# Kernel optimization log

Hardware: AMD Instinct MI355X
Metric: run time of the kernel (lower is better)

The kernel has to match this reference:

```python
import jax, jax.numpy as jnp
import numpy as np

N_NODES = 50000
N_EDGES = 800000
DIM = 128
N_GRAPHS = 64


def gcn_layer(x, edge_index, W, b):
    """PyG GCNConv: symmetric-normalized A+I aggregation then linear."""
    n = x.shape[0]
    loop = jnp.arange(n)
    row = jnp.concatenate([edge_index[0], loop])  # source nodes (+ self loops)
    col = jnp.concatenate([edge_index[1], loop])  # target nodes (+ self loops)
    deg = jax.ops.segment_sum(jnp.ones_like(col, dtype=x.dtype), col, num_segments=n)
    dis = jnp.where(deg > 0, jax.lax.rsqrt(deg), 0.0)
    norm = dis[row] * dis[col]  # [E+N]
    h = x @ W  # [N, out]
    out = jax.ops.segment_sum(h[row] * norm[:, None], col, num_segments=n)
    return out + b


def setup_inputs() -> dict:
    key = jax.random.key(0)
    ks = jax.random.split(key, 10)
    x = jax.random.normal(ks[0], (N_NODES, DIM), dtype=jnp.float32)
    edge_index = jax.random.randint(ks[1], (2, N_EDGES), 0, N_NODES, dtype=jnp.int64)
    batch = jnp.sort(jax.random.randint(ks[2], (N_NODES,), 0, N_GRAPHS, dtype=jnp.int64))
    W1 = jax.random.normal(ks[3], (DIM, DIM), dtype=jnp.float32) * 0.05
    W2 = jax.random.normal(ks[4], (DIM, DIM), dtype=jnp.float32) * 0.05
    W3 = jax.random.normal(ks[5], (DIM, DIM), dtype=jnp.float32) * 0.05
    b1 = jnp.zeros((DIM,), jnp.float32)
    b2 = jnp.zeros((DIM,), jnp.float32)
    b3 = jnp.zeros((DIM,), jnp.float32)
    return {"x": x, "edge_index": edge_index, "batch": batch,
            "W1": W1, "b1": b1, "W2": W2, "b2": b2, "W3": W3, "b3": b3}


def reference(x, edge_index, batch, W1, b1, W2, b2, W3, b3):
    h = jax.nn.relu(gcn_layer(x, edge_index, W1, b1))
    h = jax.nn.relu(gcn_layer(h, edge_index, W2, b2))
    h = jax.nn.relu(gcn_layer(h, edge_index, W3, b3))
    # global mean pool over graphs
    s = jax.ops.segment_sum(h, batch, num_segments=N_GRAPHS)
    cnt = jax.ops.segment_sum(jnp.ones((h.shape[0],), h.dtype), batch, num_segments=N_GRAPHS)
    return s / jnp.maximum(cnt, 1.0)[:, None]
```

## Files before the change

### kernel.cpp

```cpp
#include <hip/hip_runtime.h>
#include <hip/hip_bf16.h>

#define DIM 128
#define N_GRAPHS 64
#define SSTR 136

typedef __attribute__((ext_vector_type(4))) float f32x4;
typedef __attribute__((ext_vector_type(8))) short s16x8;


__device__ __forceinline__ short bf16h(float f) {
    return __builtin_bit_cast(short, __float2bfloat16(f));
}
__device__ __forceinline__ float bf16f(unsigned short h) {
    unsigned u = ((unsigned)h) << 16;
    return __builtin_bit_cast(float, u);
}

__global__ void k_rank4(const int4* __restrict__ col4, int* __restrict__ cnt,
                        int4* __restrict__ pos4, int e4) {
    int i = blockIdx.x * blockDim.x + threadIdx.x;
    if (i >= e4) return;
    int4 c = col4[i];
    int4 p;
    p.x = atomicAdd(&cnt[c.x], 1);
    p.y = atomicAdd(&cnt[c.y], 1);
    p.z = atomicAdd(&cnt[c.z], 1);
    p.w = atomicAdd(&cnt[c.w], 1);
    pos4[i] = p;
}

__global__ __launch_bounds__(256) void k_bsum(const int* __restrict__ cnt,
                                              int* __restrict__ bsum, int n) {
    __shared__ int s[256];
    int t = threadIdx.x;
    int i = blockIdx.x * 256 + t;
    s[t] = (i < n) ? cnt[i] : 0;
    __syncthreads();
    for (int o = 128; o > 0; o >>= 1) {
        if (t < o) s[t] += s[t + o];
        __syncthreads();
    }
    if (t == 0) bsum[blockIdx.x] = s[0];
}

__global__ __launch_bounds__(256) void k_bscan(const int* __restrict__ bsum,
                                               int* __restrict__ bbase, int nb) {
    __shared__ int s[256];
    int t = threadIdx.x;
    int v = (t < nb) ? bsum[t] : 0;
    s[t] = v;
    __syncthreads();
    for (int o = 1; o < 256; o <<= 1) {
        int u = (t >= o) ? s[t - o] : 0;
        __syncthreads();
        s[t] += u;
        __syncthreads();
    }
    if (t < nb) bbase[t] = s[t] - v;
}

__global__ __launch_bounds__(256) void k_bfinal(const int* __restrict__ cnt,
        const int* __restrict__ bbase, int* __restrict__ rowptr,
        float* __restrict__ dis, int n, int e) {
    __shared__ int s[256];
    int t = threadIdx.x;
    int i = blockIdx.x * 256 + t;
    int v = (i < n) ? cnt[i] : 0;
    s[t] = v;
    __syncthreads();
    for (int o = 1; o < 256; o <<= 1) {
        int u = (t >= o) ? s[t - o] : 0;
        __syncthreads();
        s[t] += u;
        __syncthreads();
    }
    if (i < n) {
        rowptr[i] = s[t] - v + bbase[blockIdx.x];
        dis[i] = rsqrtf(1.0f + (float)v);
        if (i == n - 1) rowptr[n] = e;
    }
}

__global__ void k_scat4(const int4* __restrict__ row4, const int4* __restrict__ col4,
                        const int4* __restrict__ pos4, const int* __restrict__ rowptr,
                        int* __restrict__ csr_src, int e4) {
    int i = blockIdx.x * blockDim.x + threadIdx.x;
    if (i >= e4) return;
    int4 r = row4[i];
    int4 c = col4[i];
    int4 p = pos4[i];
    csr_src[rowptr[c.x] + p.x] = r.x;
    csr_src[rowptr[c.y] + p.y] = r.y;
    csr_src[rowptr[c.z] + p.z] = r.z;
    csr_src[rowptr[c.w] + p.w] = r.w;
}


__global__ void k_cvt(const float* __restrict__ x, unsigned short* __restrict__ xb,
                      int total4) {
    int i = blockIdx.x * blockDim.x + threadIdx.x;
    if (i >= total4) return;
    float4 v = ((const float4*)x)[i];
    ushort4 o = {(unsigned short)bf16h(v.x), (unsigned short)bf16h(v.y),
                 (unsigned short)bf16h(v.z), (unsigned short)bf16h(v.w)};
    ((ushort4*)xb)[i] = o;
}


__global__ __launch_bounds__(256) void k_gcn_agg_bf(const unsigned short* __restrict__ in,
        const int* __restrict__ csr_src, const int* __restrict__ rowptr,
        const float* __restrict__ dis, float* __restrict__ agg, int n) {
    int wid = (blockIdx.x * blockDim.x + threadIdx.x) >> 6;
    if (wid >= n) return;
    int lane = threadIdx.x & 63;
    const int coff = lane * 2;
    float d = dis[wid];
    float dd = d * d;
    ushort2 sv = *(const ushort2*)&in[(size_t)wid * DIM + coff];
    float2 acc = {bf16f(sv.x) * dd, bf16f(sv.y) * dd};
    int p = rowptr[wid], p1 = rowptr[wid + 1];
    for (; p + 3 < p1; p += 4) {
        int s0 = csr_src[p], s1 = csr_src[p + 1], s2 = csr_src[p + 2], s3 = csr_src[p + 3];
        float w0 = d * dis[s0], w1 = d * dis[s1], w2 = d * dis[s2], w3 = d * dis[s3];
        ushort2 v0 = *(const ushort2*)&in[(size_t)s0 * DIM + coff];
        ushort2 v1 = *(const ushort2*)&in[(size_t)s1 * DIM + coff];
        ushort2 v2 = *(const ushort2*)&in[(size_t)s2 * DIM + coff];
        ushort2 v3 = *(const ushort2*)&in[(size_t)s3 * DIM + coff];
        acc.x += bf16f(v0.x) * w0; acc.y += bf16f(v0.y) * w0;
        acc.x += bf16f(v1.x) * w1; acc.y += bf16f(v1.y) * w1;
        acc.x += bf16f(v2.x) * w2; acc.y += bf16f(v2.y) * w2;
        acc.x += bf16f(v3.x) * w3; acc.y += bf16f(v3.y) * w3;
    }
    for (; p < p1; p++) {
        int s = csr_src[p];
        float w = d * dis[s];
        ushort2 v = *(const ushort2*)&in[(size_t)s * DIM + coff];
        acc.x += bf16f(v.x) * w;
        acc.y += bf16f(v.y) * w;
    }
    *(float2*)&agg[(size_t)wid * DIM + coff] = acc;
}

__global__ __launch_bounds__(256) void k_wprep3(
        const float* __restrict__ W1, const float* __restrict__ W2,
        const float* __restrict__ W3,
        unsigned short* __restrict__ hi1, unsigned short* __restrict__ lo1,
        unsigned short* __restrict__ hi2, unsigned short* __restrict__ lo2,
        unsigned short* __restrict__ hi3, unsigned short* __restrict__ lo3) {
    int m = blockIdx.x >> 6;
    int i = (blockIdx.x & 63) * 256 + threadIdx.x;
    const float* W = (m == 0) ? W1 : (m == 1) ? W2 : W3;
    unsigned short* hi = (m == 0) ? hi1 : (m == 1) ? hi2 : hi3;
    unsigned short* lo = (m == 0) ? lo1 : (m == 1) ? lo2 : lo3;
    int k = i >> 7, c = i & 127;
    float w = W[i];
    short h = bf16h(w);
    short l = bf16h(w - bf16f((unsigned short)h));
    hi[c * DIM + k] = (unsigned short)h;
    lo[c * DIM + k] = (unsigned short)l;
}


__global__ __launch_bounds__(256) void k_mm_mfma(
        const float* __restrict__ A, const unsigned short* __restrict__ wt_hi,
        const unsigned short* __restrict__ wt_lo, const float* __restrict__ bias,
        unsigned short* __restrict__ out, int n) {
    __shared__ unsigned short sAh[64 * SSTR];
    __shared__ unsigned short sAl[64 * SSTR];
    int tid = threadIdx.x;
    int wave = tid >> 6, lane = tid & 63;
    int r0b = blockIdx.x * 64;

    {
        int subrow = tid >> 5;
        int colb = (tid & 31) * 4;
        const float4* A4 = (const float4*)A;
#pragma unroll
        for (int j = 0; j < 8; j++) {
            int row = j * 8 + subrow;
            int rowg = r0b + row;
            int rowc = rowg < n ? rowg : (n - 1);
            float4 v = A4[(size_t)rowc * 32 + (colb >> 2)];
            short h0 = bf16h(v.x), h1 = bf16h(v.y), h2 = bf16h(v.z), h3 = bf16h(v.w);
            short l0 = bf16h(v.x - bf16f((unsigned short)h0));
            short l1 = bf16h(v.y - bf16f((unsigned short)h1));
            short l2 = bf16h(v.z - bf16f((unsigned short)h2));
            short l3 = bf16h(v.w - bf16f((unsigned short)h3));
            ushort4 hv = {(unsigned short)h0, (unsigned short)h1,
                          (unsigned short)h2, (unsigned short)h3};
            ushort4 lv = {(unsigned short)l0, (unsigned short)l1,
                          (unsigned short)l2, (unsigned short)l3};
            *(ushort4*)&sAh[row * SSTR + colb] = hv;
            *(ushort4*)&sAl[row * SSTR + colb] = lv;
        }
    }
    __syncthreads();

    int lrow = lane & 15;
    int lk = lane >> 4;
    bool full = (r0b + 64 <= n);

#pragma unroll
    for (int cti = 0; cti < 2; cti++) {
        int ct = wave * 2 + cti;
        int col = ct * 16 + lrow;
        const unsigned short* bh_base = wt_hi + (size_t)col * DIM + lk * 8;
        const unsigned short* bl_base = wt_lo + (size_t)col * DIM + lk * 8;
        s16x8 bh[4], bl[4];
#pragma unroll
        for (int ks = 0; ks < 4; ks++) {
            bh[ks] = *(const s16x8*)(bh_base + ks * 32);
            bl[ks] = *(const s16x8*)(bl_base + ks * 32);
        }
        float bcol = bias[col];

#pragma unroll
        for (int rt = 0; rt < 4; rt++) {
            const unsigned short* ah_base = &sAh[(rt * 16 + lrow) * SSTR + lk * 8];
            const unsigned short* al_base = &sAl[(rt * 16 + lrow) * SSTR + lk * 8];
            s16x8 ah[4], al[4];
#pragma unroll
            for (int ks = 0; ks < 4; ks++) {
                ah[ks] = *(const s16x8*)(ah_base + ks * 32);
                al[ks] = *(const s16x8*)(al_base + ks * 32);
            }
            f32x4 c = {0.f, 0.f, 0.f, 0.f};
#pragma unroll
            for (int ks = 0; ks < 4; ks++) {
                c = __builtin_amdgcn_mfma_f32_16x16x32_bf16(ah[ks], bh[ks], c, 0, 0, 0);
                c = __builtin_amdgcn_mfma_f32_16x16x32_bf16(al[ks], bh[ks], c, 0, 0, 0);
                c = __builtin_amdgcn_mfma_f32_16x16x32_bf16(ah[ks], bl[ks], c, 0, 0, 0);
            }
            int rbase = r0b + rt * 16 + lk * 4;
            if (full) {
#pragma unroll
                for (int reg = 0; reg < 4; reg++) {
                    float v = c[reg] + bcol;
                    v = v > 0.f ? v : 0.f;
                    out[(size_t)(rbase + reg) * DIM + col] = (unsigned short)bf16h(v);
                }
            } else {
#pragma unroll
                for (int reg = 0; reg < 4; reg++) {
                    if (rbase + reg < n) {
                        float v = c[reg] + bcol;
                        v = v > 0.f ? v : 0.f;
                        out[(size_t)(rbase + reg) * DIM + col] = (unsigned short)bf16h(v);
                    }
                }
            }
        }
    }
}


__global__ __launch_bounds__(256) void k_pool_part(const unsigned short* __restrict__ h,
        const int* __restrict__ batch, float* __restrict__ part, int n) {
    int g = blockIdx.x >> 4, s = blockIdx.x & 15;
    int lo = 0, hi = n;
    while (lo < hi) { int m = (lo + hi) >> 1; if (batch[m] < g) lo = m + 1; else hi = m; }
    int start = lo;
    int lo2 = start, hi2 = n;
    while (lo2 < hi2) { int m = (lo2 + hi2) >> 1; if (batch[m] < g + 1) lo2 = m + 1; else hi2 = m; }
    int end = lo2;

    int t = threadIdx.x;
    int wave = t >> 6, lane = t & 63;
    float2 acc = {0.f, 0.f};
    for (int r = start + s + 16 * wave; r < end; r += 64) {
        ushort2 v = *(const ushort2*)&h[(size_t)r * DIM + lane * 2];
        acc.x += bf16f(v.x); acc.y += bf16f(v.y);
    }
    __shared__ float2 red[4][64];
    red[wave][lane] = acc;
    __syncthreads();
    if (t < 64) {
        float2 s0 = red[0][t], s1 = red[1][t], s2 = red[2][t], s3 = red[3][t];
        float2 o;
        o.x = s0.x + s1.x + s2.x + s3.x;
        o.y = s0.y + s1.y + s2.y + s3.y;
        *(float2*)&part[(size_t)blockIdx.x * DIM + t * 2] = o;
    }
}

__global__ __launch_bounds__(128) void k_pool_fin(const float* __restrict__ part,
        const int* __restrict__ batch, float* __restrict__ out, int n) {
    int g = blockIdx.x, c = threadIdx.x;
    int lo = 0, hi = n;
    while (lo < hi) { int m = (lo + hi) >> 1; if (batch[m] < g) lo = m + 1; else hi = m; }
    int start = lo;
    int lo2 = start, hi2 = n;
    while (lo2 < hi2) { int m = (lo2 + hi2) >> 1; if (batch[m] < g + 1) lo2 = m + 1; else hi2 = m; }
    int end = lo2;

    float s = 0.f;
#pragma unroll
    for (int k = 0; k < 16; k++) s += part[(size_t)(g * 16 + k) * DIM + c];
    float cnt = (float)(end - start);
    cnt = cnt > 1.f ? cnt : 1.f;
    out[g * DIM + c] = s / cnt;
}


extern "C" void kernel_launch(void* const* d_in, const int* in_sizes, int n_in,
                              void* d_out, int out_size, void* d_ws, size_t ws_size,
                              hipStream_t stream) {
    const float* x  = (const float*)d_in[0];
    const int*   ei = (const int*)d_in[1];
    const int*   batch = (const int*)d_in[2];
    const float* W1 = (const float*)d_in[3];
    const float* b1 = (const float*)d_in[4];
    const float* W2 = (const float*)d_in[5];
    const float* b2 = (const float*)d_in[6];
    const float* W3 = (const float*)d_in[7];
    const float* b3 = (const float*)d_in[8];

    int n = in_sizes[0] / DIM;
    int e = in_sizes[1] / 2;
    const int* erow = ei;
    const int* ecol = ei + e;
    int e4 = e / 4;
    int nb = (n + 255) / 256;

    char* ws = (char*)d_ws;
    size_t off = 0;
    auto alloc = [&](size_t bytes) -> void* {
        void* p = (void*)(ws + off);
        off += (bytes + 255) & ~(size_t)255;
        return p;
    };
    float* dis     = (float*)alloc((size_t)n * 4);
    int*   rowptr  = (int*)alloc((size_t)(n + 1) * 4);
    int*   csr_src = (int*)alloc((size_t)e * 4);
    float* agg     = (float*)alloc((size_t)n * DIM * 4);
    unsigned short* xb    = (unsigned short*)alloc((size_t)n * DIM * 2);
    unsigned short* hbufA = (unsigned short*)alloc((size_t)n * DIM * 2);
    unsigned short* hbufB = (unsigned short*)alloc((size_t)n * DIM * 2);
    unsigned short* wt_hi1 = (unsigned short*)alloc(DIM * DIM * 2);
    unsigned short* wt_lo1 = (unsigned short*)alloc(DIM * DIM * 2);
    unsigned short* wt_hi2 = (unsigned short*)alloc(DIM * DIM * 2);
    unsigned short* wt_lo2 = (unsigned short*)alloc(DIM * DIM * 2);
    unsigned short* wt_hi3 = (unsigned short*)alloc(DIM * DIM * 2);
    unsigned short* wt_lo3 = (unsigned short*)alloc(DIM * DIM * 2);
    float* part    = (float*)alloc((size_t)1024 * DIM * 4);
    int*   pos     = (int*)alloc((size_t)e * 4);
    int* cnt    = (int*)agg;
    int* bsum   = ((int*)agg) + n;
    int* bbase  = ((int*)agg) + n + 256;

    hipMemsetAsync(cnt, 0, (size_t)n * 4, stream);
    k_rank4<<<(e4 + 255) / 256, 256, 0, stream>>>((const int4*)ecol, cnt, (int4*)pos, e4);
    k_bsum<<<nb, 256, 0, stream>>>(cnt, bsum, n);
    k_bscan<<<1, 256, 0, stream>>>(bsum, bbase, nb);
    k_bfinal<<<nb, 256, 0, stream>>>(cnt, bbase, rowptr, dis, n, e);
    k_scat4<<<(e4 + 255) / 256, 256, 0, stream>>>((const int4*)erow, (const int4*)ecol,
                                                  (const int4*)pos, rowptr, csr_src, e4);

    int total4 = n * DIM / 4;
    k_cvt<<<(total4 + 255) / 256, 256, 0, stream>>>(x, xb, total4);
    k_wprep3<<<192, 256, 0, stream>>>(W1, W2, W3, wt_hi1, wt_lo1, wt_hi2, wt_lo2,
                                      wt_hi3, wt_lo3);

    dim3 aggGrid(((size_t)n * 64 + 255) / 256);
    dim3 mmGrid((n + 63) / 64);

    k_gcn_agg_bf<<<aggGrid, 256, 0, stream>>>(xb, csr_src, rowptr, dis, agg, n);
    k_mm_mfma<<<mmGrid, 256, 0, stream>>>(agg, wt_hi1, wt_lo1, b1, hbufA, n);
    k_gcn_agg_bf<<<aggGrid, 256, 0, stream>>>(hbufA, csr_src, rowptr, dis, agg, n);
    k_mm_mfma<<<mmGrid, 256, 0, stream>>>(agg, wt_hi2, wt_lo2, b2, hbufB, n);
    k_gcn_agg_bf<<<aggGrid, 256, 0, stream>>>(hbufB, csr_src, rowptr, dis, agg, n);
    k_mm_mfma<<<mmGrid, 256, 0, stream>>>(agg, wt_hi3, wt_lo3, b3, hbufA, n);

    k_pool_part<<<1024, 256, 0, stream>>>(hbufA, batch, part, n);
    k_pool_fin<<<N_GRAPHS, 128, 0, stream>>>(part, batch, (float*)d_out, n);
}
```

Before: 257.2 us.

## Reorder GCN layer to transform-then-aggregate with bf16 intermediates

Each layer now multiplies by W before the sparse aggregation instead of after. The aggregation kernel takes over the bias, ReLU and bf16 store, and the matmul reads bf16 inputs directly. This removes the fp32 agg buffer and its write and read, and drops one of the three split-bf16 MFMA passes since A is now bf16 only. In exchange, the matmul output Y is rounded to bf16 before aggregation, which adds precision loss.

```diff
diff --git a/kernel.cpp b/kernel.cpp
--- a/kernel.cpp
+++ b/kernel.cpp
@@ -107,10 +107,98 @@
     ((ushort4*)xb)[i] = o;
 }
 
+__global__ __launch_bounds__(256) void k_wprep3(
+        const float* __restrict__ W1, const float* __restrict__ W2,
+        const float* __restrict__ W3,
+        unsigned short* __restrict__ hi1, unsigned short* __restrict__ lo1,
+        unsigned short* __restrict__ hi2, unsigned short* __restrict__ lo2,
+        unsigned short* __restrict__ hi3, unsigned short* __restrict__ lo3) {
+    int m = blockIdx.x >> 6;
+    int i = (blockIdx.x & 63) * 256 + threadIdx.x;
+    const float* W = (m == 0) ? W1 : (m == 1) ? W2 : W3;
+    unsigned short* hi = (m == 0) ? hi1 : (m == 1) ? hi2 : hi3;
+    unsigned short* lo = (m == 0) ? lo1 : (m == 1) ? lo2 : lo3;
+    int k = i >> 7, c = i & 127;
+    float w = W[i];
+    short h = bf16h(w);
+    short l = bf16h(w - bf16f((unsigned short)h));
+    hi[c * DIM + k] = (unsigned short)h;
+    lo[c * DIM + k] = (unsigned short)l;
+}
+
+
+__global__ __launch_bounds__(256) void k_mm2(
+        const unsigned short* __restrict__ A, const unsigned short* __restrict__ wt_hi,
+        const unsigned short* __restrict__ wt_lo, unsigned short* __restrict__ out, int n) {
+    __shared__ unsigned short sA[64 * SSTR];
+    int tid = threadIdx.x;
+    int wave = tid >> 6, lane = tid & 63;
+    int r0b = blockIdx.x * 64;
+
+    for (int c = tid; c < 1024; c += 256) {
+        int row = c >> 4;
+        int cc = (c & 15) * 8;
+        int rowg = r0b + row;
+        int rowc = rowg < n ? rowg : (n - 1);
+        s16x8 v = *(const s16x8*)&A[(size_t)rowc * DIM + cc];
+        *(s16x8*)&sA[row * SSTR + cc] = v;
+    }
+    __syncthreads();
+
+    int lrow = lane & 15;
+    int lk = lane >> 4;
+    bool full = (r0b + 64 <= n);
+
+#pragma unroll
+    for (int cti = 0; cti < 2; cti++) {
+        int ct = wave * 2 + cti;
+        int col = ct * 16 + lrow;
+        const unsigned short* bh_base = wt_hi + (size_t)col * DIM + lk * 8;
+        const unsigned short* bl_base = wt_lo + (size_t)col * DIM + lk * 8;
+        s16x8 bh[4], bl[4];
+#pragma unroll
+        for (int ks = 0; ks < 4; ks++) {
+            bh[ks] = *(const s16x8*)(bh_base + ks * 32);
+            bl[ks] = *(const s16x8*)(bl_base + ks * 32);
+        }
+
+#pragma unroll
+        for (int rt = 0; rt < 4; rt++) {
+            const unsigned short* a_base = &sA[(rt * 16 + lrow) * SSTR + lk * 8];
+            s16x8 a[4];
+#pragma unroll
+            for (int ks = 0; ks < 4; ks++) {
+                a[ks] = *(const s16x8*)(a_base + ks * 32);
+            }
+            f32x4 c = {0.f, 0.f, 0.f, 0.f};
+#pragma unroll
+            for (int ks = 0; ks < 4; ks++) {
+                c = __builtin_amdgcn_mfma_f32_16x16x32_bf16(a[ks], bh[ks], c, 0, 0, 0);
+                c = __builtin_amdgcn_mfma_f32_16x16x32_bf16(a[ks], bl[ks], c, 0, 0, 0);
+            }
+            int rbase = r0b + rt * 16 + lk * 4;
+            if (full) {
+#pragma unroll
+                for (int reg = 0; reg < 4; reg++) {
+                    out[(size_t)(rbase + reg) * DIM + col] = (unsigned short)bf16h(c[reg]);
+                }
+            } else {
+#pragma unroll
+                for (int reg = 0; reg < 4; reg++) {
+                    if (rbase + reg < n) {
+                        out[(size_t)(rbase + reg) * DIM + col] = (unsigned short)bf16h(c[reg]);
+                    }
+                }
+            }
+        }
+    }
+}
+
 
 __global__ __launch_bounds__(256) void k_gcn_agg_bf(const unsigned short* __restrict__ in,
         const int* __restrict__ csr_src, const int* __restrict__ rowptr,
-        const float* __restrict__ dis, float* __restrict__ agg, int n) {
+        const float* __restrict__ dis, const float* __restrict__ bias,
+        unsigned short* __restrict__ hout, int n) {
     int wid = (blockIdx.x * blockDim.x + threadIdx.x) >> 6;
     if (wid >= n) return;
     int lane = threadIdx.x & 63;
@@ -139,119 +227,13 @@
         acc.x += bf16f(v.x) * w;
         acc.y += bf16f(v.y) * w;
     }
-    *(float2*)&agg[(size_t)wid * DIM + coff] = acc;
-}
-
-__global__ __launch_bounds__(256) void k_wprep3(
-        const float* __restrict__ W1, const float* __restrict__ W2,
-        const float* __restrict__ W3,
-        unsigned short* __restrict__ hi1, unsigned short* __restrict__ lo1,
-        unsigned short* __restrict__ hi2, unsigned short* __restrict__ lo2,
-        unsigned short* __restrict__ hi3, unsigned short* __restrict__ lo3) {
-    int m = blockIdx.x >> 6;
-    int i = (blockIdx.x & 63) * 256 + threadIdx.x;
-    const float* W = (m == 0) ? W1 : (m == 1) ? W2 : W3;
-    unsigned short* hi = (m == 0) ? hi1 : (m == 1) ? hi2 : hi3;
-    unsigned short* lo = (m == 0) ? lo1 : (m == 1) ? lo2 : lo3;
-    int k = i >> 7, c = i & 127;
-    float w = W[i];
-    short h = bf16h(w);
-    short l = bf16h(w - bf16f((unsigned short)h));
-    hi[c * DIM + k] = (unsigned short)h;
-    lo[c * DIM + k] = (unsigned short)l;
-}
-
-
-__global__ __launch_bounds__(256) void k_mm_mfma(
-        const float* __restrict__ A, const unsigned short* __restrict__ wt_hi,
-        const unsigned short* __restrict__ wt_lo, const float* __restrict__ bias,
-        unsigned short* __restrict__ out, int n) {
-    __shared__ unsigned short sAh[64 * SSTR];
-    __shared__ unsigned short sAl[64 * SSTR];
-    int tid = threadIdx.x;
-    int wave = tid >> 6, lane = tid & 63;
-    int r0b = blockIdx.x * 64;
-
-    {
-        int subrow = tid >> 5;
-        int colb = (tid & 31) * 4;
-        const float4* A4 = (const float4*)A;
-#pragma unroll
-        for (int j = 0; j < 8; j++) {
-            int row = j * 8 + subrow;
-            int rowg = r0b + row;
-            int rowc = rowg < n ? rowg : (n - 1);
-            float4 v = A4[(size_t)rowc * 32 + (colb >> 2)];
-            short h0 = bf16h(v.x), h1 = bf16h(v.y), h2 = bf16h(v.z), h3 = bf16h(v.w);
-            short l0 = bf16h(v.x - bf16f((unsigned short)h0));
-            short l1 = bf16h(v.y - bf16f((unsigned short)h1));
-            short l2 = bf16h(v.z - bf16f((unsigned short)h2));
-            short l3 = bf16h(v.w - bf16f((unsigned short)h3));
-            ushort4 hv = {(unsigned short)h0, (unsigned short)h1,
-                          (unsigned short)h2, (unsigned short)h3};
-            ushort4 lv = {(unsigned short)l0, (unsigned short)l1,
-                          (unsigned short)l2, (unsigned short)l3};
-            *(ushort4*)&sAh[row * SSTR + colb] = hv;
-            *(ushort4*)&sAl[row * SSTR + colb] = lv;
-        }
-    }
-    __syncthreads();
-
-    int lrow = lane & 15;
-    int lk = lane >> 4;
-    bool full = (r0b + 64 <= n);
-
-#pragma unroll
-    for (int cti = 0; cti < 2; cti++) {
-        int ct = wave * 2 + cti;
-        int col = ct * 16 + lrow;
-        const unsigned short* bh_base = wt_hi + (size_t)col * DIM + lk * 8;
-        const unsigned short* bl_base = wt_lo + (size_t)col * DIM + lk * 8;
-        s16x8 bh[4], bl[4];
-#pragma unroll
-        for (int ks = 0; ks < 4; ks++) {
-            bh[ks] = *(const s16x8*)(bh_base + ks * 32);
-            bl[ks] = *(const s16x8*)(bl_base + ks * 32);
-        }
-        float bcol = bias[col];
-
-#pragma unroll
-        for (int rt = 0; rt < 4; rt++) {
-            const unsigned short* ah_base = &sAh[(rt * 16 + lrow) * SSTR + lk * 8];
-            const unsigned short* al_base = &sAl[(rt * 16 + lrow) * SSTR + lk * 8];
-            s16x8 ah[4], al[4];
-#pragma unroll
-            for (int ks = 0; ks < 4; ks++) {
-                ah[ks] = *(const s16x8*)(ah_base + ks * 32);
-                al[ks] = *(const s16x8*)(al_base + ks * 32);
-            }
-            f32x4 c = {0.f, 0.f, 0.f, 0.f};
-#pragma unroll
-            for (int ks = 0; ks < 4; ks++) {
-                c = __builtin_amdgcn_mfma_f32_16x16x32_bf16(ah[ks], bh[ks], c, 0, 0, 0);
-                c = __builtin_amdgcn_mfma_f32_16x16x32_bf16(al[ks], bh[ks], c, 0, 0, 0);
-                c = __builtin_amdgcn_mfma_f32_16x16x32_bf16(ah[ks], bl[ks], c, 0, 0, 0);
-            }
-            int rbase = r0b + rt * 16 + lk * 4;
-            if (full) {
-#pragma unroll
-                for (int reg = 0; reg < 4; reg++) {
-                    float v = c[reg] + bcol;
-                    v = v > 0.f ? v : 0.f;
-                    out[(size_t)(rbase + reg) * DIM + col] = (unsigned short)bf16h(v);
-                }
-            } else {
-#pragma unroll
-                for (int reg = 0; reg < 4; reg++) {
-                    if (rbase + reg < n) {
-                        float v = c[reg] + bcol;
-                        v = v > 0.f ? v : 0.f;
-                        out[(size_t)(rbase + reg) * DIM + col] = (unsigned short)bf16h(v);
-                    }
-                }
-            }
-        }
-    }
+    float2 bv = *(const float2*)&bias[coff];
+    float ox = acc.x + bv.x;
+    float oy = acc.y + bv.y;
+    ox = ox > 0.f ? ox : 0.f;
+    oy = oy > 0.f ? oy : 0.f;
+    ushort2 o = {(unsigned short)bf16h(ox), (unsigned short)bf16h(oy)};
+    *(ushort2*)&hout[(size_t)wid * DIM + coff] = o;
 }
 
 
@@ -333,10 +315,10 @@
     float* dis     = (float*)alloc((size_t)n * 4);
     int*   rowptr  = (int*)alloc((size_t)(n + 1) * 4);
     int*   csr_src = (int*)alloc((size_t)e * 4);
-    float* agg     = (float*)alloc((size_t)n * DIM * 4);
-    unsigned short* xb    = (unsigned short*)alloc((size_t)n * DIM * 2);
-    unsigned short* hbufA = (unsigned short*)alloc((size_t)n * DIM * 2);
-    unsigned short* hbufB = (unsigned short*)alloc((size_t)n * DIM * 2);
+    unsigned short* xb  = (unsigned short*)alloc((size_t)n * DIM * 2);
+    unsigned short* Y   = (unsigned short*)alloc((size_t)n * DIM * 2);
+    unsigned short* hA  = (unsigned short*)alloc((size_t)n * DIM * 2);
+    unsigned short* hB  = (unsigned short*)alloc((size_t)n * DIM * 2);
     unsigned short* wt_hi1 = (unsigned short*)alloc(DIM * DIM * 2);
     unsigned short* wt_lo1 = (unsigned short*)alloc(DIM * DIM * 2);
     unsigned short* wt_hi2 = (unsigned short*)alloc(DIM * DIM * 2);
@@ -345,9 +327,9 @@
     unsigned short* wt_lo3 = (unsigned short*)alloc(DIM * DIM * 2);
     float* part    = (float*)alloc((size_t)1024 * DIM * 4);
     int*   pos     = (int*)alloc((size_t)e * 4);
-    int* cnt    = (int*)agg;
-    int* bsum   = ((int*)agg) + n;
-    int* bbase  = ((int*)agg) + n + 256;
+    int* cnt    = (int*)Y;
+    int* bsum   = ((int*)Y) + n;
+    int* bbase  = ((int*)Y) + n + 256;
 
     hipMemsetAsync(cnt, 0, (size_t)n * 4, stream);
     k_rank4<<<(e4 + 255) / 256, 256, 0, stream>>>((const int4*)ecol, cnt, (int4*)pos, e4);
@@ -365,13 +347,13 @@
     dim3 aggGrid(((size_t)n * 64 + 255) / 256);
     dim3 mmGrid((n + 63) / 64);
 
-    k_gcn_agg_bf<<<aggGrid, 256, 0, stream>>>(xb, csr_src, rowptr, dis, agg, n);
-    k_mm_mfma<<<mmGrid, 256, 0, stream>>>(agg, wt_hi1, wt_lo1, b1, hbufA, n);
-    k_gcn_agg_bf<<<aggGrid, 256, 0, stream>>>(hbufA, csr_src, rowptr, dis, agg, n);
-    k_mm_mfma<<<mmGrid, 256, 0, stream>>>(agg, wt_hi2, wt_lo2, b2, hbufB, n);
-    k_gcn_agg_bf<<<aggGrid, 256, 0, stream>>>(hbufB, csr_src, rowptr, dis, agg, n);
-    k_mm_mfma<<<mmGrid, 256, 0, stream>>>(agg, wt_hi3, wt_lo3, b3, hbufA, n);
-
-    k_pool_part<<<1024, 256, 0, stream>>>(hbufA, batch, part, n);
+    k_mm2<<<mmGrid, 256, 0, stream>>>(xb, wt_hi1, wt_lo1, Y, n);
+    k_gcn_agg_bf<<<aggGrid, 256, 0, stream>>>(Y, csr_src, rowptr, dis, b1, hA, n);
+    k_mm2<<<mmGrid, 256, 0, stream>>>(hA, wt_hi2, wt_lo2, Y, n);
+    k_gcn_agg_bf<<<aggGrid, 256, 0, stream>>>(Y, csr_src, rowptr, dis, b2, hB, n);
+    k_mm2<<<mmGrid, 256, 0, stream>>>(hB, wt_hi3, wt_lo3, Y, n);
+    k_gcn_agg_bf<<<aggGrid, 256, 0, stream>>>(Y, csr_src, rowptr, dis, b3, hA, n);
+
+    k_pool_part<<<1024, 256, 0, stream>>>(hA, batch, part, n);
     k_pool_fin<<<N_GRAPHS, 128, 0, stream>>>(part, batch, (float*)d_out, n);
 }
```

After: 261.1 us. Within noise of the previous version (+1.5%).
